# Optimization experiments

Measured on AMD Instinct MI355X. Metric: run time of the kernel, lower is better.

## Reference

```python
import jax, jax.numpy as jnp
import numpy as np

NUM_FEATURES = 256
NUM_PIDS = 5554          # must equal hardcoded FocalLoss ignore_index
NUM_CQ = 50000
N_ROIS = 2048
OIM_SCALAR = 30.0
IGNORE_INDEX = 5554
ALPHA = 1.0
GAMMA = 2.0


def _l2norm(x):
    return x / jnp.linalg.norm(x, axis=-1, keepdims=True)


def setup_inputs() -> dict:
    key = jax.random.key(0)
    k1, k2, k3, k4, k5 = jax.random.split(key, 5)
    inputs = _l2norm(jax.random.normal(k1, (N_ROIS, NUM_FEATURES), jnp.float32))
    # targets >= 1 so label = targets-1 >= 0 (the inds filter is all-True -> static shapes)
    # targets == NUM_PIDS+1 -> label == NUM_PIDS == ignore_index (unlabeled, ignored in loss)
    targets = jax.random.randint(k2, (N_ROIS,), 1, NUM_PIDS + 2, dtype=jnp.int64)
    ious = jax.random.uniform(k3, (N_ROIS,), jnp.float32)
    lut = _l2norm(jax.random.normal(k4, (NUM_PIDS, NUM_FEATURES), jnp.float32))
    cq = _l2norm(jax.random.normal(k5, (NUM_CQ, NUM_FEATURES), jnp.float32))
    return {"inputs": inputs, "lut": lut, "cq": cq, "targets": targets, "ious": ious}


def _focal_loss(logits, labels):
    # F.cross_entropy(reduction='none', ignore_index=IGNORE_INDEX) then
    # focal = alpha * (1-pt)^gamma * ce, mean over ALL samples (ignored -> 0).
    logp = jax.nn.log_softmax(logits, axis=-1)                       # [N, C]
    ce = -jnp.take_along_axis(logp, labels[:, None], axis=1)[:, 0]   # [N]
    ce = jnp.where(labels == IGNORE_INDEX, 0.0, ce)
    pt = jnp.exp(-ce)
    return jnp.mean(ALPHA * (1.0 - pt) ** GAMMA * ce)


def reference(inputs, lut, cq, targets, ious):
    # targets = cat(roi_label); label = targets - 1; inds all True by construction.
    label = targets - 1
    # LOIM forward: logits against labeled LUT and unlabeled circular queue.
    table = jnp.concatenate([lut, cq], axis=0)          # [P+Q, D]
    projected = OIM_SCALAR * (inputs @ table.T)         # [N, P+Q]
    loss_oim = _focal_loss(projected, label)
    return loss_oim, inputs, label
```

## Files before the change

### kernel.cpp

```cpp
#include <hip/hip_runtime.h>
#include <hip/hip_bf16.h>


#define NFEAT 256
#define NROIS 2048
#define NPIDS 5554
#define NCLS 55554
#define NCHUNKS 3473
#define NCH32 1737
#define NCLSP (NCH32 * 32)
#define S2F 43.280851226668906f
#define LN2F 0.6931471805599453f
#define LOFF 524289

typedef float f32x4 __attribute__((ext_vector_type(4)));
typedef short bf16x8 __attribute__((ext_vector_type(8)));
typedef unsigned short u16x8 __attribute__((ext_vector_type(8)));

#if __has_builtin(__builtin_amdgcn_exp2f)
#define EXP2(x) __builtin_amdgcn_exp2f(x)
#else
#define EXP2(x) exp2f(x)
#endif

__device__ __forceinline__ short bfb(float x) {
    return __builtin_bit_cast(short, __float2bfloat16(x));
}

__device__ __forceinline__ void gll16(const void* g, void* l) {
    __builtin_amdgcn_global_load_lds(
        (const __attribute__((address_space(1))) void*)g,
        (__attribute__((address_space(3))) void*)l, 16, 0, 0);
}

__global__ __launch_bounds__(256) void preprocess(
        const float* __restrict__ inputs, const float* __restrict__ lut,
        const float* __restrict__ cq, const int* __restrict__ cand0,
        const int* __restrict__ cand1, unsigned short* __restrict__ tb,
        unsigned short* __restrict__ ab, int* __restrict__ lab,
        float* __restrict__ S, float* __restrict__ f, const int useTB) {
    const int tid = threadIdx.x;
    const int bx = blockIdx.x;

    if (bx == 0) {
        __shared__ int smode;
        __shared__ const int* sT;
        if (tid == 0) {
            const int* T = cand0;
            const unsigned u0 = (unsigned)cand0[0];
            const float f0 = __builtin_bit_cast(float, cand0[0]);
            const bool oki = (u0 >= 1u && u0 <= 6000u);
            const bool okf = (f0 >= 1.0f && f0 <= 6000.0f);
            if (!oki && !okf) T = cand1;
            int mode = 0;
            const unsigned tu0 = (unsigned)T[0];
            const float tf0 = __builtin_bit_cast(float, T[0]);
            if (tu0 >= 1u && tu0 <= 6000u) mode = ((T[1] | T[3] | T[5] | T[7]) == 0) ? 1 : 0;
            else if (tf0 >= 1.0f && tf0 <= 6000.0f) mode = 2;
            smode = mode; sT = T;
        }
        __syncthreads();
        const int mode = smode;
        const int* T = sT;
        for (int j = tid; j < NROIS; j += 256) {
            int tv;
            if (mode == 1)      tv = T[2 * j];
            else if (mode == 2) tv = (int)__builtin_bit_cast(float, T[j]);
            else                tv = T[j];
            const int lv = tv - 1;
            lab[j] = lv;
            f[LOFF + j] = __bfloat162float(__float2bfloat16((float)lv));
        }
        for (int j = tid; j < NROIS + 8; j += 256) S[j] = 0.0f;
    }

    if (bx < 512) {
        const int i = bx * 256 + tid;
        const float4 v = *reinterpret_cast<const float4*>(inputs + (size_t)i * 4);
        float* o = f + 1 + (size_t)i * 4;
        o[0] = v.x; o[1] = v.y; o[2] = v.z; o[3] = v.w;
        if (useTB) {
            ushort4 u;
            u.x = (unsigned short)bfb(v.x); u.y = (unsigned short)bfb(v.y);
            u.z = (unsigned short)bfb(v.z); u.w = (unsigned short)bfb(v.w);
            *reinterpret_cast<ushort4*>(ab + (size_t)i * 4) = u;
        }
    }

    if (useTB) {
        const size_t LUTN = (size_t)NPIDS * NFEAT;
        const size_t TOT  = (size_t)NCLS * NFEAT;
        const size_t TOTP = (size_t)NCLSP * NFEAT;
        const size_t stride = (size_t)gridDim.x * 256 * 8;
        for (size_t e = ((size_t)bx * 256 + tid) * 8; e < TOTP; e += stride) {
            u16x8 o = {0, 0, 0, 0, 0, 0, 0, 0};
            if (e < TOT) {
                const float* sp = (e < LUTN) ? (lut + e) : (cq + (e - LUTN));
                const float4 a = *reinterpret_cast<const float4*>(sp);
                const float4 b = *reinterpret_cast<const float4*>(sp + 4);
                o[0] = (unsigned short)bfb(a.x); o[1] = (unsigned short)bfb(a.y);
                o[2] = (unsigned short)bfb(a.z); o[3] = (unsigned short)bfb(a.w);
                o[4] = (unsigned short)bfb(b.x); o[5] = (unsigned short)bfb(b.y);
                o[6] = (unsigned short)bfb(b.z); o[7] = (unsigned short)bfb(b.w);
            }
            *reinterpret_cast<u16x8*>(tb + e) = o;
        }
    }
}

template <bool TB>
__global__ __launch_bounds__(256, 2) void main_gemm4(const float* __restrict__ inputs,
                                                     const unsigned short* __restrict__ tb,
                                                     const unsigned short* __restrict__ ab,
                                                     const float* __restrict__ lut,
                                                     const float* __restrict__ cq,
                                                     float* __restrict__ S) {
    __shared__ short ldsb[3][8192];
    const int tid = threadIdx.x;
    const int lane = tid & 63;
    const int wave = tid >> 6;
    const int cs = blockIdx.x & 63;
    const int rg = blockIdx.x >> 6;
    const int rowbase = rg * 256 + wave * 64;
    const int li = lane & 15;
    const int q = lane >> 4;
    const int xorli = 4 * (li & 7);

    bf16x8 afrag[4][8];
    if constexpr (TB) {
        #pragma unroll
        for (int s = 0; s < 4; s++) {
            const unsigned short* rp = ab + (size_t)(rowbase + s * 16 + li) * NFEAT + q * 8;
            #pragma unroll
            for (int kc = 0; kc < 8; kc++)
                afrag[s][kc] = *reinterpret_cast<const bf16x8*>(rp + kc * 32);
        }
    } else {
        #pragma unroll
        for (int s = 0; s < 4; s++) {
            const float* rp = inputs + (size_t)(rowbase + s * 16 + li) * NFEAT + q * 8;
            #pragma unroll
            for (int kc = 0; kc < 8; kc++) {
                const float4 x0 = *reinterpret_cast<const float4*>(rp + kc * 32);
                const float4 x1 = *reinterpret_cast<const float4*>(rp + kc * 32 + 4);
                bf16x8 a;
                a[0] = bfb(x0.x); a[1] = bfb(x0.y); a[2] = bfb(x0.z); a[3] = bfb(x0.w);
                a[4] = bfb(x1.x); a[5] = bfb(x1.y); a[6] = bfb(x1.z); a[7] = bfb(x1.w);
                afrag[s][kc] = a;
            }
        }
    }

    float sums[4][4] = {{0.f,0.f,0.f,0.f},{0.f,0.f,0.f,0.f},
                        {0.f,0.f,0.f,0.f},{0.f,0.f,0.f,0.f}};
    char* const lbase = (char*)&ldsb[0][0];

    if constexpr (TB) {
        const int cc0 = tid >> 5;
        const int uo = ((tid & 31) ^ (4 * (cc0 & 7))) * 8;
        const int ldd = wave * 1024;
        const int cA = (cs * NCH32) >> 6;
        const int cB = ((cs + 1) * NCH32) >> 6;
        const int NB = cB - cA;
        const unsigned short* psrc = tb + (size_t)(cA * 32 + cc0) * NFEAT + uo;
        int ob0 = 0, ob1 = 16384, ob2 = 32768;

        #pragma unroll
        for (int k = 0; k < 4; k++)
            gll16(psrc + (size_t)(8 * k) * NFEAT, lbase + ob0 + ldd + k * 4096);
        psrc += (size_t)32 * NFEAT;
        if (NB > 1) {
            #pragma unroll
            for (int k = 0; k < 4; k++)
                gll16(psrc + (size_t)(8 * k) * NFEAT, lbase + ob1 + ldd + k * 4096);
            psrc += (size_t)32 * NFEAT;
        }

        for (int i = 0; i < NB; ++i) {
            if (i + 1 < NB) asm volatile("s_waitcnt vmcnt(4)\n\ts_barrier" ::: "memory");
            else            asm volatile("s_waitcnt vmcnt(0)\n\ts_barrier" ::: "memory");
            if (i + 2 < NB) {
                #pragma unroll
                for (int k = 0; k < 4; k++)
                    gll16(psrc + (size_t)(8 * k) * NFEAT, lbase + ob2 + ldd + k * 4096);
                psrc += (size_t)32 * NFEAT;
            }
            #pragma unroll
            for (int h = 0; h < 2; h++) {
                const int cc = h * 16 + li;
                bf16x8 bfr[8];
                #pragma unroll
                for (int kc = 0; kc < 8; kc++) {
                    const int slot = cc * 32 + ((q + 4 * kc) ^ xorli);
                    bfr[kc] = *reinterpret_cast<const bf16x8*>(lbase + ob0 + slot * 16);
                }
                f32x4 acc[4] = {{0.f,0.f,0.f,0.f},{0.f,0.f,0.f,0.f},
                                {0.f,0.f,0.f,0.f},{0.f,0.f,0.f,0.f}};
                __builtin_amdgcn_s_setprio(1);
                #pragma unroll
                for (int kc = 0; kc < 8; kc++) {
                    acc[0] = __builtin_amdgcn_mfma_f32_16x16x32_bf16(afrag[0][kc], bfr[kc], acc[0], 0, 0, 0);
                    acc[1] = __builtin_amdgcn_mfma_f32_16x16x32_bf16(afrag[1][kc], bfr[kc], acc[1], 0, 0, 0);
                    acc[2] = __builtin_amdgcn_mfma_f32_16x16x32_bf16(afrag[2][kc], bfr[kc], acc[2], 0, 0, 0);
                    acc[3] = __builtin_amdgcn_mfma_f32_16x16x32_bf16(afrag[3][kc], bfr[kc], acc[3], 0, 0, 0);
                }
                __builtin_amdgcn_s_setprio(0);
                #pragma unroll
                for (int s = 0; s < 4; s++)
                    #pragma unroll
                    for (int r = 0; r < 4; r++)
                        sums[s][r] += EXP2(S2F * acc[s][r] - S2F);
            }
            const int t = ob0; ob0 = ob1; ob1 = ob2; ob2 = t;
        }
    } else {
        short* fb = (short*)lbase;
        const int s0 = tid, s1 = tid + 256;
        const int cc0 = s0 >> 5, cc1 = s1 >> 5;
        const int uo0 = ((s0 & 31) ^ (4 * (cc0 & 7))) * 8;
        const int uo1 = ((s1 & 31) ^ (4 * (cc1 & 7))) * 8;
        const int cA = (cs * NCHUNKS) >> 6;
        const int cB = ((cs + 1) * NCHUNKS) >> 6;
        {
            int n0 = cA * 16 + cc0; n0 = n0 < (NCLS - 1) ? n0 : (NCLS - 1);
            int n1 = cA * 16 + cc1; n1 = n1 < (NCLS - 1) ? n1 : (NCLS - 1);
            const float* r0 = ((n0 < NPIDS) ? lut + (size_t)n0 * NFEAT
                                            : cq + (size_t)(n0 - NPIDS) * NFEAT) + uo0;
            const float* r1 = ((n1 < NPIDS) ? lut + (size_t)n1 * NFEAT
                                            : cq + (size_t)(n1 - NPIDS) * NFEAT) + uo1;
            const float4 a0 = *reinterpret_cast<const float4*>(r0);
            const float4 a1 = *reinterpret_cast<const float4*>(r0 + 4);
            const float4 b0 = *reinterpret_cast<const float4*>(r1);
            const float4 b1 = *reinterpret_cast<const float4*>(r1 + 4);
            bf16x8 v0, v1;
            v0[0]=bfb(a0.x); v0[1]=bfb(a0.y); v0[2]=bfb(a0.z); v0[3]=bfb(a0.w);
            v0[4]=bfb(a1.x); v0[5]=bfb(a1.y); v0[6]=bfb(a1.z); v0[7]=bfb(a1.w);
            v1[0]=bfb(b0.x); v1[1]=bfb(b0.y); v1[2]=bfb(b0.z); v1[3]=bfb(b0.w);
            v1[4]=bfb(b1.x); v1[5]=bfb(b1.y); v1[6]=bfb(b1.z); v1[7]=bfb(b1.w);
            *reinterpret_cast<bf16x8*>(&fb[s0 * 8]) = v0;
            *reinterpret_cast<bf16x8*>(&fb[s1 * 8]) = v1;
        }
        __syncthreads();
        int cur = 0;
        for (int ci = cA; ci < cB; ++ci) {
            const bool pf = (ci + 1 < cB);
            float4 f0a, f0b, f1a, f1b;
            if (pf) {
                int n0 = (ci + 1) * 16 + cc0; n0 = n0 < (NCLS - 1) ? n0 : (NCLS - 1);
                int n1 = (ci + 1) * 16 + cc1; n1 = n1 < (NCLS - 1) ? n1 : (NCLS - 1);
                const float* r0 = ((n0 < NPIDS) ? lut + (size_t)n0 * NFEAT
                                                : cq + (size_t)(n0 - NPIDS) * NFEAT) + uo0;
                const float* r1 = ((n1 < NPIDS) ? lut + (size_t)n1 * NFEAT
                                                : cq + (size_t)(n1 - NPIDS) * NFEAT) + uo1;
                f0a = *reinterpret_cast<const float4*>(r0);
                f0b = *reinterpret_cast<const float4*>(r0 + 4);
                f1a = *reinterpret_cast<const float4*>(r1);
                f1b = *reinterpret_cast<const float4*>(r1 + 4);
            }
            f32x4 acc[4] = {{0.f,0.f,0.f,0.f},{0.f,0.f,0.f,0.f},
                            {0.f,0.f,0.f,0.f},{0.f,0.f,0.f,0.f}};
            #pragma unroll
            for (int kc = 0; kc < 8; kc++) {
                const int slot = li * 32 + ((q + 4 * kc) ^ xorli);
                const bf16x8 b = *reinterpret_cast<const bf16x8*>(&fb[cur * 4096 + slot * 8]);
                acc[0] = __builtin_amdgcn_mfma_f32_16x16x32_bf16(afrag[0][kc], b, acc[0], 0, 0, 0);
                acc[1] = __builtin_amdgcn_mfma_f32_16x16x32_bf16(afrag[1][kc], b, acc[1], 0, 0, 0);
                acc[2] = __builtin_amdgcn_mfma_f32_16x16x32_bf16(afrag[2][kc], b, acc[2], 0, 0, 0);
                acc[3] = __builtin_amdgcn_mfma_f32_16x16x32_bf16(afrag[3][kc], b, acc[3], 0, 0, 0);
            }
            const float valid = ((ci * 16 + li) < NCLS) ? 1.0f : 0.0f;
            #pragma unroll
            for (int s = 0; s < 4; s++)
                #pragma unroll
                for (int r = 0; r < 4; r++)
                    sums[s][r] += valid * EXP2(S2F * (acc[s][r] - 1.0f));
            if (pf) {
                bf16x8 p0, p1;
                p0[0]=bfb(f0a.x); p0[1]=bfb(f0a.y); p0[2]=bfb(f0a.z); p0[3]=bfb(f0a.w);
                p0[4]=bfb(f0b.x); p0[5]=bfb(f0b.y); p0[6]=bfb(f0b.z); p0[7]=bfb(f0b.w);
                p1[0]=bfb(f1a.x); p1[1]=bfb(f1a.y); p1[2]=bfb(f1a.z); p1[3]=bfb(f1a.w);
                p1[4]=bfb(f1b.x); p1[5]=bfb(f1b.y); p1[6]=bfb(f1b.z); p1[7]=bfb(f1b.w);
                *reinterpret_cast<bf16x8*>(&fb[(cur ^ 1) * 4096 + s0 * 8]) = p0;
                *reinterpret_cast<bf16x8*>(&fb[(cur ^ 1) * 4096 + s1 * 8]) = p1;
            }
            __syncthreads();
            cur ^= 1;
        }
    }

    #pragma unroll
    for (int s = 0; s < 4; s++)
        #pragma unroll
        for (int r = 0; r < 4; r++) {
            float v = sums[s][r];
            v += __shfl_xor(v, 1); v += __shfl_xor(v, 2);
            v += __shfl_xor(v, 4); v += __shfl_xor(v, 8);
            sums[s][r] = v;
        }
    if (li == 0) {
        #pragma unroll
        for (int s = 0; s < 4; s++)
            #pragma unroll
            for (int r = 0; r < 4; r++)
                atomicAdd(&S[rowbase + s * 16 + q * 4 + r], sums[s][r]);
    }
}

__global__ __launch_bounds__(256) void focal_final(const float* __restrict__ inputs,
                                                   const float* __restrict__ lut,
                                                   const int* __restrict__ lab,
                                                   const float* __restrict__ S,
                                                   float* __restrict__ loss_acc,
                                                   unsigned int* __restrict__ cnt,
                                                   float* __restrict__ f) {
    const int wave = threadIdx.x >> 6;
    const int lane = threadIdx.x & 63;
    const int row = blockIdx.x * 4 + wave;
    const int label = lab[row];
    const bool valid = (label >= 0 && label < NPIDS);
    const int lr = valid ? label : 0;
    const float4 a = *reinterpret_cast<const float4*>(inputs + (size_t)row * NFEAT + lane * 4);
    const float4 b = *reinterpret_cast<const float4*>(lut + (size_t)lr * NFEAT + lane * 4);
    float v = a.x * b.x + a.y * b.y + a.z * b.z + a.w * b.w;
    #pragma unroll
    for (int m = 1; m < 64; m <<= 1) v += __shfl_xor(v, m);

    __shared__ float red[4];
    if (lane == 0) {
        float fo = 0.0f;
        if (valid) {
            const float l2 = v * S2F;
            const float lse2 = S2F + log2f(S[row]);
            float ce = fmaxf((lse2 - l2) * LN2F, 0.0f);
            const float pt = EXP2(l2 - lse2);
            const float om = 1.0f - pt;
            fo = om * om * ce;
        }
        red[wave] = fo;
    }
    __syncthreads();
    if (threadIdx.x == 0) {
        atomicAdd(loss_acc, red[0] + red[1] + red[2] + red[3]);
        __threadfence();
        const unsigned done = atomicAdd(cnt, 1u) + 1u;
        if (done == gridDim.x) {
            const float tot = atomicAdd(loss_acc, 0.0f);
            f[0] = tot * (1.0f / NROIS);
        }
    }
}

extern "C" void kernel_launch(void* const* d_in, const int* in_sizes, int n_in,
                              void* d_out, int out_size, void* d_ws, size_t ws_size,
                              hipStream_t stream) {
    const float* inputs = (const float*)d_in[0];
    const float* lut    = (const float*)d_in[1];
    const float* cq     = (const float*)d_in[2];
    const int*   cand0  = (const int*)d_in[3];
    const int*   cand1  = (const int*)((n_in > 4) ? d_in[4] : d_in[3]);
    float* f = (float*)d_out;

    const size_t TBB = (size_t)NCLSP * NFEAT * 2;
    const size_t ABB = (size_t)NROIS * NFEAT * 2;
    char* ws = (char*)d_ws;
    const bool useTB = ws_size >= TBB + ABB + 32768;

    unsigned short* tb = useTB ? (unsigned short*)ws : nullptr;
    unsigned short* ab = useTB ? (unsigned short*)(ws + TBB) : nullptr;
    float* S = useTB ? (float*)(ws + TBB + ABB) : (float*)ws;
    float* loss_acc    = S + NROIS;
    unsigned int* cnt  = (unsigned int*)(S + NROIS + 1);
    int* lab           = (int*)(S + NROIS + 8);

    preprocess<<<useTB ? 4096 : 512, 256, 0, stream>>>(inputs, lut, cq, cand0, cand1,
                                                       tb, ab, lab, S, f, useTB ? 1 : 0);
    if (useTB) main_gemm4<true><<<512, 256, 0, stream>>>(inputs, tb, ab, lut, cq, S);
    else       main_gemm4<false><<<512, 256, 0, stream>>>(inputs, tb, ab, lut, cq, S);
    focal_final<<<512, 256, 0, stream>>>(inputs, lut, lab, S, loss_acc, cnt, f);
}
```

Measured before the change: 171.5 us.

## Switch bf16 GEMM tile to 32x32x16 MFMA with new LDS swizzle

The workspace-backed path now uses 32x32x16 bf16 MFMA instructions instead of 16x16x32. Each wave holds two 32-row A fragments over 16 K-chunks, and the LDS XOR swizzle and B-fragment indexing are changed to match the new lane layout. The row-sum reduction is updated for 32-lane groups. This is meant to cut instruction count and LDS reads per FLOP, at the cost of more accumulator registers and different bank-conflict behaviour.

```diff
diff --git a/kernel.cpp b/kernel.cpp
--- a/kernel.cpp
+++ b/kernel.cpp
@@ -14,6 +14,7 @@
 #define LOFF 524289
 
 typedef float f32x4 __attribute__((ext_vector_type(4)));
+typedef float f32x16 __attribute__((ext_vector_type(16)));
 typedef short bf16x8 __attribute__((ext_vector_type(8)));
 typedef unsigned short u16x8 __attribute__((ext_vector_type(8)));
 
@@ -109,7 +110,7 @@
 }
 
 template <bool TB>
-__global__ __launch_bounds__(256, 2) void main_gemm4(const float* __restrict__ inputs,
+__global__ __launch_bounds__(256, 2) void main_gemm5(const float* __restrict__ inputs,
                                                      const unsigned short* __restrict__ tb,
                                                      const unsigned short* __restrict__ ab,
                                                      const float* __restrict__ lut,
@@ -122,20 +123,110 @@
     const int cs = blockIdx.x & 63;
     const int rg = blockIdx.x >> 6;
     const int rowbase = rg * 256 + wave * 64;
-    const int li = lane & 15;
-    const int q = lane >> 4;
-    const int xorli = 4 * (li & 7);
-
-    bf16x8 afrag[4][8];
+    char* const lbase = (char*)&ldsb[0][0];
+
     if constexpr (TB) {
-        #pragma unroll
-        for (int s = 0; s < 4; s++) {
-            const unsigned short* rp = ab + (size_t)(rowbase + s * 16 + li) * NFEAT + q * 8;
-            #pragma unroll
-            for (int kc = 0; kc < 8; kc++)
-                afrag[s][kc] = *reinterpret_cast<const bf16x8*>(rp + kc * 32);
+        const int cc = lane & 31;
+        const int p  = lane >> 5;
+        const int xc = 2 * (cc & 3);
+
+        bf16x8 afrag[2][16];
+        #pragma unroll
+        for (int s = 0; s < 2; s++) {
+            const unsigned short* rp = ab + (size_t)(rowbase + s * 32 + cc) * NFEAT + p * 8;
+            #pragma unroll
+            for (int kc = 0; kc < 16; kc++)
+                afrag[s][kc] = *reinterpret_cast<const bf16x8*>(rp + kc * 16);
+        }
+
+        float sums[2][16];
+        #pragma unroll
+        for (int s = 0; s < 2; s++)
+            #pragma unroll
+            for (int r = 0; r < 16; r++) sums[s][r] = 0.0f;
+
+        const int cc0 = tid >> 5;
+        const int uo = ((tid & 31) ^ (2 * (cc0 & 3))) * 8;
+        const int ldd = wave * 1024;
+        const int cA = (cs * NCH32) >> 6;
+        const int cB = ((cs + 1) * NCH32) >> 6;
+        const int NB = cB - cA;
+        const unsigned short* psrc = tb + (size_t)(cA * 32 + cc0) * NFEAT + uo;
+        int ob0 = 0, ob1 = 16384, ob2 = 32768;
+
+        #pragma unroll
+        for (int k = 0; k < 4; k++)
+            gll16(psrc + (size_t)(8 * k) * NFEAT, lbase + ob0 + ldd + k * 4096);
+        psrc += (size_t)32 * NFEAT;
+        if (NB > 1) {
+            #pragma unroll
+            for (int k = 0; k < 4; k++)
+                gll16(psrc + (size_t)(8 * k) * NFEAT, lbase + ob1 + ldd + k * 4096);
+            psrc += (size_t)32 * NFEAT;
+        }
+
+        for (int i = 0; i < NB; ++i) {
+            if (i + 1 < NB) asm volatile("s_waitcnt vmcnt(4)\n\ts_barrier" ::: "memory");
+            else            asm volatile("s_waitcnt vmcnt(0)\n\ts_barrier" ::: "memory");
+            if (i + 2 < NB) {
+                #pragma unroll
+                for (int k = 0; k < 4; k++)
+                    gll16(psrc + (size_t)(8 * k) * NFEAT, lbase + ob2 + ldd + k * 4096);
+                psrc += (size_t)32 * NFEAT;
+            }
+            f32x16 acc0 = {0.f,0.f,0.f,0.f,0.f,0.f,0.f,0.f,
+                           0.f,0.f,0.f,0.f,0.f,0.f,0.f,0.f};
+            f32x16 acc1 = {0.f,0.f,0.f,0.f,0.f,0.f,0.f,0.f,
+                           0.f,0.f,0.f,0.f,0.f,0.f,0.f,0.f};
+            #pragma unroll
+            for (int h = 0; h < 2; h++) {
+                bf16x8 bfr[8];
+                #pragma unroll
+                for (int j = 0; j < 8; j++) {
+                    const int kc = h * 8 + j;
+                    const int slot = cc * 32 + ((2 * kc + p) ^ xc);
+                    bfr[j] = *reinterpret_cast<const bf16x8*>(lbase + ob0 + slot * 16);
+                }
+                __builtin_amdgcn_s_setprio(1);
+                #pragma unroll
+                for (int j = 0; j < 8; j++) {
+                    acc0 = __builtin_amdgcn_mfma_f32_32x32x16_bf16(afrag[0][h * 8 + j], bfr[j], acc0, 0, 0, 0);
+                    acc1 = __builtin_amdgcn_mfma_f32_32x32x16_bf16(afrag[1][h * 8 + j], bfr[j], acc1, 0, 0, 0);
+                }
+                __builtin_amdgcn_s_setprio(0);
+            }
+            #pragma unroll
+            for (int r = 0; r < 16; r++) {
+                sums[0][r] += EXP2(S2F * acc0[r] - S2F);
+                sums[1][r] += EXP2(S2F * acc1[r] - S2F);
+            }
+            const int t = ob0; ob0 = ob1; ob1 = ob2; ob2 = t;
+        }
+
+        #pragma unroll
+        for (int s = 0; s < 2; s++)
+            #pragma unroll
+            for (int r = 0; r < 16; r++) {
+                float v = sums[s][r];
+                v += __shfl_xor(v, 1); v += __shfl_xor(v, 2);
+                v += __shfl_xor(v, 4); v += __shfl_xor(v, 8);
+                v += __shfl_xor(v, 16);
+                sums[s][r] = v;
+            }
+        if (cc == 0) {
+            #pragma unroll
+            for (int s = 0; s < 2; s++)
+                #pragma unroll
+                for (int r = 0; r < 16; r++) {
+                    const int row = rowbase + s * 32 + (r & 3) + 8 * (r >> 2) + 4 * p;
+                    atomicAdd(&S[row], sums[s][r]);
+                }
         }
     } else {
+        const int li = lane & 15;
+        const int q = lane >> 4;
+        const int xorli = 4 * (li & 7);
+        bf16x8 afrag[4][8];
         #pragma unroll
         for (int s = 0; s < 4; s++) {
             const float* rp = inputs + (size_t)(rowbase + s * 16 + li) * NFEAT + q * 8;
@@ -149,71 +240,8 @@
                 afrag[s][kc] = a;
             }
         }
-    }
-
-    float sums[4][4] = {{0.f,0.f,0.f,0.f},{0.f,0.f,0.f,0.f},
-                        {0.f,0.f,0.f,0.f},{0.f,0.f,0.f,0.f}};
-    char* const lbase = (char*)&ldsb[0][0];
-
-    if constexpr (TB) {
-        const int cc0 = tid >> 5;
-        const int uo = ((tid & 31) ^ (4 * (cc0 & 7))) * 8;
-        const int ldd = wave * 1024;
-        const int cA = (cs * NCH32) >> 6;
-        const int cB = ((cs + 1) * NCH32) >> 6;
-        const int NB = cB - cA;
-        const unsigned short* psrc = tb + (size_t)(cA * 32 + cc0) * NFEAT + uo;
-        int ob0 = 0, ob1 = 16384, ob2 = 32768;
-
-        #pragma unroll
-        for (int k = 0; k < 4; k++)
-            gll16(psrc + (size_t)(8 * k) * NFEAT, lbase + ob0 + ldd + k * 4096);
-        psrc += (size_t)32 * NFEAT;
-        if (NB > 1) {
-            #pragma unroll
-            for (int k = 0; k < 4; k++)
-                gll16(psrc + (size_t)(8 * k) * NFEAT, lbase + ob1 + ldd + k * 4096);
-            psrc += (size_t)32 * NFEAT;
-        }
-
-        for (int i = 0; i < NB; ++i) {
-            if (i + 1 < NB) asm volatile("s_waitcnt vmcnt(4)\n\ts_barrier" ::: "memory");
-            else            asm volatile("s_waitcnt vmcnt(0)\n\ts_barrier" ::: "memory");
-            if (i + 2 < NB) {
-                #pragma unroll
-                for (int k = 0; k < 4; k++)
-                    gll16(psrc + (size_t)(8 * k) * NFEAT, lbase + ob2 + ldd + k * 4096);
-                psrc += (size_t)32 * NFEAT;
-            }
-            #pragma unroll
-            for (int h = 0; h < 2; h++) {
-                const int cc = h * 16 + li;
-                bf16x8 bfr[8];
-                #pragma unroll
-                for (int kc = 0; kc < 8; kc++) {
-                    const int slot = cc * 32 + ((q + 4 * kc) ^ xorli);
-                    bfr[kc] = *reinterpret_cast<const bf16x8*>(lbase + ob0 + slot * 16);
-                }
-                f32x4 acc[4] = {{0.f,0.f,0.f,0.f},{0.f,0.f,0.f,0.f},
-                                {0.f,0.f,0.f,0.f},{0.f,0.f,0.f,0.f}};
-                __builtin_amdgcn_s_setprio(1);
-                #pragma unroll
-                for (int kc = 0; kc < 8; kc++) {
-                    acc[0] = __builtin_amdgcn_mfma_f32_16x16x32_bf16(afrag[0][kc], bfr[kc], acc[0], 0, 0, 0);
-                    acc[1] = __builtin_amdgcn_mfma_f32_16x16x32_bf16(afrag[1][kc], bfr[kc], acc[1], 0, 0, 0);
-                    acc[2] = __builtin_amdgcn_mfma_f32_16x16x32_bf16(afrag[2][kc], bfr[kc], acc[2], 0, 0, 0);
-                    acc[3] = __builtin_amdgcn_mfma_f32_16x16x32_bf16(afrag[3][kc], bfr[kc], acc[3], 0, 0, 0);
-                }
-                __builtin_amdgcn_s_setprio(0);
-                #pragma unroll
-                for (int s = 0; s < 4; s++)
-                    #pragma unroll
-                    for (int r = 0; r < 4; r++)
-                        sums[s][r] += EXP2(S2F * acc[s][r] - S2F);
-            }
-            const int t = ob0; ob0 = ob1; ob1 = ob2; ob2 = t;
-        }
-    } else {
+        float sums[4][4] = {{0.f,0.f,0.f,0.f},{0.f,0.f,0.f,0.f},
+                            {0.f,0.f,0.f,0.f},{0.f,0.f,0.f,0.f}};
         short* fb = (short*)lbase;
         const int s0 = tid, s1 = tid + 256;
         const int cc0 = s0 >> 5, cc1 = s1 >> 5;
@@ -286,23 +314,22 @@
             __syncthreads();
             cur ^= 1;
         }
-    }
-
-    #pragma unroll
-    for (int s = 0; s < 4; s++)
-        #pragma unroll
-        for (int r = 0; r < 4; r++) {
-            float v = sums[s][r];
-            v += __shfl_xor(v, 1); v += __shfl_xor(v, 2);
-            v += __shfl_xor(v, 4); v += __shfl_xor(v, 8);
-            sums[s][r] = v;
-        }
-    if (li == 0) {
         #pragma unroll
         for (int s = 0; s < 4; s++)
             #pragma unroll
-            for (int r = 0; r < 4; r++)
-                atomicAdd(&S[rowbase + s * 16 + q * 4 + r], sums[s][r]);
+            for (int r = 0; r < 4; r++) {
+                float v = sums[s][r];
+                v += __shfl_xor(v, 1); v += __shfl_xor(v, 2);
+                v += __shfl_xor(v, 4); v += __shfl_xor(v, 8);
+                sums[s][r] = v;
+            }
+        if (li == 0) {
+            #pragma unroll
+            for (int s = 0; s < 4; s++)
+                #pragma unroll
+                for (int r = 0; r < 4; r++)
+                    atomicAdd(&S[rowbase + s * 16 + q * 4 + r], sums[s][r]);
+        }
     }
 }
 
@@ -374,7 +401,7 @@
 
     preprocess<<<useTB ? 4096 : 512, 256, 0, stream>>>(inputs, lut, cq, cand0, cand1,
                                                        tb, ab, lab, S, f, useTB ? 1 : 0);
-    if (useTB) main_gemm4<true><<<512, 256, 0, stream>>>(inputs, tb, ab, lut, cq, S);
-    else       main_gemm4<false><<<512, 256, 0, stream>>>(inputs, tb, ab, lut, cq, S);
+    if (useTB) main_gemm5<true><<<512, 256, 0, stream>>>(inputs, tb, ab, lut, cq, S);
+    else       main_gemm5<false><<<512, 256, 0, stream>>>(inputs, tb, ab, lut, cq, S);
     focal_final<<<512, 256, 0, stream>>>(inputs, lut, lab, S, loss_acc, cnt, f);
 }
```

After: 190.8 us. 11.2% more time.

## Use 512-thread blocks with 32 rows per wave in fused GEMM

Applied to the files above, without the earlier changes.

The main GEMM+exp kernel now runs 8 waves per block, each owning 32 rows instead of 64. Each wave keeps half as many A fragments and accumulators, and the cooperative LDS loads are split across twice as many threads. The goal is to cut register pressure and raise occupancy (launch bounds 512,4) so latency is hidden better. The cost is that each LDS B-fragment read now feeds only 2 MFMAs instead of 4, which doubles LDS read traffic per FLOP and halves per-wave reuse.

```diff
diff --git a/kernel.cpp b/kernel.cpp
--- a/kernel.cpp
+++ b/kernel.cpp
@@ -109,7 +109,7 @@
 }
 
 template <bool TB>
-__global__ __launch_bounds__(256, 2) void main_gemm4(const float* __restrict__ inputs,
+__global__ __launch_bounds__(512, 4) void main_gemm6(const float* __restrict__ inputs,
                                                      const unsigned short* __restrict__ tb,
                                                      const unsigned short* __restrict__ ab,
                                                      const float* __restrict__ lut,
@@ -121,15 +121,16 @@
     const int wave = tid >> 6;
     const int cs = blockIdx.x & 63;
     const int rg = blockIdx.x >> 6;
-    const int rowbase = rg * 256 + wave * 64;
+    const int rowbase = rg * 256 + wave * 32;
     const int li = lane & 15;
     const int q = lane >> 4;
     const int xorli = 4 * (li & 7);
-
-    bf16x8 afrag[4][8];
+    char* const lbase = (char*)&ldsb[0][0];
+
+    bf16x8 afrag[2][8];
     if constexpr (TB) {
         #pragma unroll
-        for (int s = 0; s < 4; s++) {
+        for (int s = 0; s < 2; s++) {
             const unsigned short* rp = ab + (size_t)(rowbase + s * 16 + li) * NFEAT + q * 8;
             #pragma unroll
             for (int kc = 0; kc < 8; kc++)
@@ -137,7 +138,7 @@
         }
     } else {
         #pragma unroll
-        for (int s = 0; s < 4; s++) {
+        for (int s = 0; s < 2; s++) {
             const float* rp = inputs + (size_t)(rowbase + s * 16 + li) * NFEAT + q * 8;
             #pragma unroll
             for (int kc = 0; kc < 8; kc++) {
@@ -151,9 +152,7 @@
         }
     }
 
-    float sums[4][4] = {{0.f,0.f,0.f,0.f},{0.f,0.f,0.f,0.f},
-                        {0.f,0.f,0.f,0.f},{0.f,0.f,0.f,0.f}};
-    char* const lbase = (char*)&ldsb[0][0];
+    float sums[2][4] = {{0.f,0.f,0.f,0.f},{0.f,0.f,0.f,0.f}};
 
     if constexpr (TB) {
         const int cc0 = tid >> 5;
@@ -165,24 +164,21 @@
         const unsigned short* psrc = tb + (size_t)(cA * 32 + cc0) * NFEAT + uo;
         int ob0 = 0, ob1 = 16384, ob2 = 32768;
 
-        #pragma unroll
-        for (int k = 0; k < 4; k++)
-            gll16(psrc + (size_t)(8 * k) * NFEAT, lbase + ob0 + ldd + k * 4096);
+        gll16(psrc, lbase + ob0 + ldd);
+        gll16(psrc + (size_t)16 * NFEAT, lbase + ob0 + 8192 + ldd);
         psrc += (size_t)32 * NFEAT;
         if (NB > 1) {
-            #pragma unroll
-            for (int k = 0; k < 4; k++)
-                gll16(psrc + (size_t)(8 * k) * NFEAT, lbase + ob1 + ldd + k * 4096);
+            gll16(psrc, lbase + ob1 + ldd);
+            gll16(psrc + (size_t)16 * NFEAT, lbase + ob1 + 8192 + ldd);
             psrc += (size_t)32 * NFEAT;
         }
 
         for (int i = 0; i < NB; ++i) {
-            if (i + 1 < NB) asm volatile("s_waitcnt vmcnt(4)\n\ts_barrier" ::: "memory");
+            if (i + 1 < NB) asm volatile("s_waitcnt vmcnt(2)\n\ts_barrier" ::: "memory");
             else            asm volatile("s_waitcnt vmcnt(0)\n\ts_barrier" ::: "memory");
             if (i + 2 < NB) {
-                #pragma unroll
-                for (int k = 0; k < 4; k++)
-                    gll16(psrc + (size_t)(8 * k) * NFEAT, lbase + ob2 + ldd + k * 4096);
+                gll16(psrc, lbase + ob2 + ldd);
+                gll16(psrc + (size_t)16 * NFEAT, lbase + ob2 + 8192 + ldd);
                 psrc += (size_t)32 * NFEAT;
             }
             #pragma unroll
@@ -194,19 +190,16 @@
                     const int slot = cc * 32 + ((q + 4 * kc) ^ xorli);
                     bfr[kc] = *reinterpret_cast<const bf16x8*>(lbase + ob0 + slot * 16);
                 }
-                f32x4 acc[4] = {{0.f,0.f,0.f,0.f},{0.f,0.f,0.f,0.f},
-                                {0.f,0.f,0.f,0.f},{0.f,0.f,0.f,0.f}};
+                f32x4 acc[2] = {{0.f,0.f,0.f,0.f},{0.f,0.f,0.f,0.f}};
                 __builtin_amdgcn_s_setprio(1);
                 #pragma unroll
                 for (int kc = 0; kc < 8; kc++) {
                     acc[0] = __builtin_amdgcn_mfma_f32_16x16x32_bf16(afrag[0][kc], bfr[kc], acc[0], 0, 0, 0);
                     acc[1] = __builtin_amdgcn_mfma_f32_16x16x32_bf16(afrag[1][kc], bfr[kc], acc[1], 0, 0, 0);
-                    acc[2] = __builtin_amdgcn_mfma_f32_16x16x32_bf16(afrag[2][kc], bfr[kc], acc[2], 0, 0, 0);
-                    acc[3] = __builtin_amdgcn_mfma_f32_16x16x32_bf16(afrag[3][kc], bfr[kc], acc[3], 0, 0, 0);
                 }
                 __builtin_amdgcn_s_setprio(0);
                 #pragma unroll
-                for (int s = 0; s < 4; s++)
+                for (int s = 0; s < 2; s++)
                     #pragma unroll
                     for (int r = 0; r < 4; r++)
                         sums[s][r] += EXP2(S2F * acc[s][r] - S2F);
@@ -215,73 +208,52 @@
         }
     } else {
         short* fb = (short*)lbase;
-        const int s0 = tid, s1 = tid + 256;
-        const int cc0 = s0 >> 5, cc1 = s1 >> 5;
-        const int uo0 = ((s0 & 31) ^ (4 * (cc0 & 7))) * 8;
-        const int uo1 = ((s1 & 31) ^ (4 * (cc1 & 7))) * 8;
+        const int cc0 = tid >> 5;
+        const int uo0 = ((tid & 31) ^ (4 * (cc0 & 7))) * 8;
         const int cA = (cs * NCHUNKS) >> 6;
         const int cB = ((cs + 1) * NCHUNKS) >> 6;
         {
             int n0 = cA * 16 + cc0; n0 = n0 < (NCLS - 1) ? n0 : (NCLS - 1);
-            int n1 = cA * 16 + cc1; n1 = n1 < (NCLS - 1) ? n1 : (NCLS - 1);
             const float* r0 = ((n0 < NPIDS) ? lut + (size_t)n0 * NFEAT
                                             : cq + (size_t)(n0 - NPIDS) * NFEAT) + uo0;
-            const float* r1 = ((n1 < NPIDS) ? lut + (size_t)n1 * NFEAT
-                                            : cq + (size_t)(n1 - NPIDS) * NFEAT) + uo1;
             const float4 a0 = *reinterpret_cast<const float4*>(r0);
             const float4 a1 = *reinterpret_cast<const float4*>(r0 + 4);
-            const float4 b0 = *reinterpret_cast<const float4*>(r1);
-            const float4 b1 = *reinterpret_cast<const float4*>(r1 + 4);
-            bf16x8 v0, v1;
+            bf16x8 v0;
             v0[0]=bfb(a0.x); v0[1]=bfb(a0.y); v0[2]=bfb(a0.z); v0[3]=bfb(a0.w);
             v0[4]=bfb(a1.x); v0[5]=bfb(a1.y); v0[6]=bfb(a1.z); v0[7]=bfb(a1.w);
-            v1[0]=bfb(b0.x); v1[1]=bfb(b0.y); v1[2]=bfb(b0.z); v1[3]=bfb(b0.w);
-            v1[4]=bfb(b1.x); v1[5]=bfb(b1.y); v1[6]=bfb(b1.z); v1[7]=bfb(b1.w);
-            *reinterpret_cast<bf16x8*>(&fb[s0 * 8]) = v0;
-            *reinterpret_cast<bf16x8*>(&fb[s1 * 8]) = v1;
+            *reinterpret_cast<bf16x8*>(&fb[tid * 8]) = v0;
         }
         __syncthreads();
         int cur = 0;
         for (int ci = cA; ci < cB; ++ci) {
             const bool pf = (ci + 1 < cB);
-            float4 f0a, f0b, f1a, f1b;
+            float4 f0a, f0b;
             if (pf) {
                 int n0 = (ci + 1) * 16 + cc0; n0 = n0 < (NCLS - 1) ? n0 : (NCLS - 1);
-                int n1 = (ci + 1) * 16 + cc1; n1 = n1 < (NCLS - 1) ? n1 : (NCLS - 1);
                 const float* r0 = ((n0 < NPIDS) ? lut + (size_t)n0 * NFEAT
                                                 : cq + (size_t)(n0 - NPIDS) * NFEAT) + uo0;
-                const float* r1 = ((n1 < NPIDS) ? lut + (size_t)n1 * NFEAT
-                                                : cq + (size_t)(n1 - NPIDS) * NFEAT) + uo1;
                 f0a = *reinterpret_cast<const float4*>(r0);
                 f0b = *reinterpret_cast<const float4*>(r0 + 4);
-                f1a = *reinterpret_cast<const float4*>(r1);
-                f1b = *reinterpret_cast<const float4*>(r1 + 4);
-            }
-            f32x4 acc[4] = {{0.f,0.f,0.f,0.f},{0.f,0.f,0.f,0.f},
-                            {0.f,0.f,0.f,0.f},{0.f,0.f,0.f,0.f}};
+            }
+            f32x4 acc[2] = {{0.f,0.f,0.f,0.f},{0.f,0.f,0.f,0.f}};
             #pragma unroll
             for (int kc = 0; kc < 8; kc++) {
                 const int slot = li * 32 + ((q + 4 * kc) ^ xorli);
                 const bf16x8 b = *reinterpret_cast<const bf16x8*>(&fb[cur * 4096 + slot * 8]);
                 acc[0] = __builtin_amdgcn_mfma_f32_16x16x32_bf16(afrag[0][kc], b, acc[0], 0, 0, 0);
                 acc[1] = __builtin_amdgcn_mfma_f32_16x16x32_bf16(afrag[1][kc], b, acc[1], 0, 0, 0);
-                acc[2] = __builtin_amdgcn_mfma_f32_16x16x32_bf16(afrag[2][kc], b, acc[2], 0, 0, 0);
-                acc[3] = __builtin_amdgcn_mfma_f32_16x16x32_bf16(afrag[3][kc], b, acc[3], 0, 0, 0);
             }
             const float valid = ((ci * 16 + li) < NCLS) ? 1.0f : 0.0f;
             #pragma unroll
-            for (int s = 0; s < 4; s++)
+            for (int s = 0; s < 2; s++)
                 #pragma unroll
                 for (int r = 0; r < 4; r++)
                     sums[s][r] += valid * EXP2(S2F * (acc[s][r] - 1.0f));
             if (pf) {
-                bf16x8 p0, p1;
+                bf16x8 p0;
                 p0[0]=bfb(f0a.x); p0[1]=bfb(f0a.y); p0[2]=bfb(f0a.z); p0[3]=bfb(f0a.w);
                 p0[4]=bfb(f0b.x); p0[5]=bfb(f0b.y); p0[6]=bfb(f0b.z); p0[7]=bfb(f0b.w);
-                p1[0]=bfb(f1a.x); p1[1]=bfb(f1a.y); p1[2]=bfb(f1a.z); p1[3]=bfb(f1a.w);
-                p1[4]=bfb(f1b.x); p1[5]=bfb(f1b.y); p1[6]=bfb(f1b.z); p1[7]=bfb(f1b.w);
-                *reinterpret_cast<bf16x8*>(&fb[(cur ^ 1) * 4096 + s0 * 8]) = p0;
-                *reinterpret_cast<bf16x8*>(&fb[(cur ^ 1) * 4096 + s1 * 8]) = p1;
+                *reinterpret_cast<bf16x8*>(&fb[(cur ^ 1) * 4096 + tid * 8]) = p0;
             }
             __syncthreads();
             cur ^= 1;
@@ -289,7 +261,7 @@
     }
 
     #pragma unroll
-    for (int s = 0; s < 4; s++)
+    for (int s = 0; s < 2; s++)
         #pragma unroll
         for (int r = 0; r < 4; r++) {
             float v = sums[s][r];
@@ -299,7 +271,7 @@
         }
     if (li == 0) {
         #pragma unroll
-        for (int s = 0; s < 4; s++)
+        for (int s = 0; s < 2; s++)
             #pragma unroll
             for (int r = 0; r < 4; r++)
                 atomicAdd(&S[rowbase + s * 16 + q * 4 + r], sums[s][r]);
@@ -374,7 +346,7 @@
 
     preprocess<<<useTB ? 4096 : 512, 256, 0, stream>>>(inputs, lut, cq, cand0, cand1,
                                                        tb, ab, lab, S, f, useTB ? 1 : 0);
-    if (useTB) main_gemm4<true><<<512, 256, 0, stream>>>(inputs, tb, ab, lut, cq, S);
-    else       main_gemm4<false><<<512, 256, 0, stream>>>(inputs, tb, ab, lut, cq, S);
+    if (useTB) main_gemm6<true><<<512, 512, 0, stream>>>(inputs, tb, ab, lut, cq, S);
+    else       main_gemm6<false><<<512, 512, 0, stream>>>(inputs, tb, ab, lut, cq, S);
     focal_final<<<512, 256, 0, stream>>>(inputs, lut, lab, S, loss_acc, cnt, f);
 }
```

Result: slower. 185.9 us (+8.4%).

## Fuse preprocess, GEMM and focal reduction into one cooperative kernel

Applied to the files above, without the earlier changes.

Replaces the three separate launches (bf16 conversion, GEMM with exp-sum, focal finalize) with a single cooperative kernel that uses grid-wide syncs between phases. The aim is to remove kernel launch gaps and the tail idle time between dependent kernels. In exchange, the conversion phase now runs on only 512 blocks instead of 4096, and grid syncs carry their own cost. If the cooperative launch fails, the code falls back to the old three-kernel path.

```diff
diff --git a/kernel.cpp b/kernel.cpp
--- a/kernel.cpp
+++ b/kernel.cpp
@@ -1,5 +1,8 @@
 #include <hip/hip_runtime.h>
 #include <hip/hip_bf16.h>
+#include <hip/hip_cooperative_groups.h>
+
+namespace cg = cooperative_groups;
 
 
 #define NFEAT 256
@@ -33,14 +36,18 @@
         (__attribute__((address_space(3))) void*)l, 16, 0, 0);
 }
 
-__global__ __launch_bounds__(256) void preprocess(
+__global__ __launch_bounds__(256, 2) void mega(
         const float* __restrict__ inputs, const float* __restrict__ lut,
         const float* __restrict__ cq, const int* __restrict__ cand0,
         const int* __restrict__ cand1, unsigned short* __restrict__ tb,
         unsigned short* __restrict__ ab, int* __restrict__ lab,
-        float* __restrict__ S, float* __restrict__ f, const int useTB) {
+        float* __restrict__ S, float* __restrict__ loss_acc,
+        unsigned int* __restrict__ cnt, float* __restrict__ f) {
+    __shared__ short ldsb[3][8192];
     const int tid = threadIdx.x;
     const int bx = blockIdx.x;
+    const int lane = tid & 63;
+    const int wave = tid >> 6;
 
     if (bx == 0) {
         __shared__ int smode;
@@ -73,7 +80,212 @@
         }
         for (int j = tid; j < NROIS + 8; j += 256) S[j] = 0.0f;
     }
-
+    {
+        const int i = bx * 256 + tid;
+        const float4 v = *reinterpret_cast<const float4*>(inputs + (size_t)i * 4);
+        float* o = f + 1 + (size_t)i * 4;
+        o[0] = v.x; o[1] = v.y; o[2] = v.z; o[3] = v.w;
+        ushort4 u;
+        u.x = (unsigned short)bfb(v.x); u.y = (unsigned short)bfb(v.y);
+        u.z = (unsigned short)bfb(v.z); u.w = (unsigned short)bfb(v.w);
+        *reinterpret_cast<ushort4*>(ab + (size_t)i * 4) = u;
+    }
+    {
+        const size_t LUTN = (size_t)NPIDS * NFEAT;
+        const size_t TOT  = (size_t)NCLS * NFEAT;
+        const size_t TOTP = (size_t)NCLSP * NFEAT;
+        const size_t stride = (size_t)gridDim.x * 256 * 8;
+        for (size_t e = ((size_t)bx * 256 + tid) * 8; e < TOTP; e += stride) {
+            u16x8 o = {0, 0, 0, 0, 0, 0, 0, 0};
+            if (e < TOT) {
+                const float* sp = (e < LUTN) ? (lut + e) : (cq + (e - LUTN));
+                const float4 a = *reinterpret_cast<const float4*>(sp);
+                const float4 b = *reinterpret_cast<const float4*>(sp + 4);
+                o[0] = (unsigned short)bfb(a.x); o[1] = (unsigned short)bfb(a.y);
+                o[2] = (unsigned short)bfb(a.z); o[3] = (unsigned short)bfb(a.w);
+                o[4] = (unsigned short)bfb(b.x); o[5] = (unsigned short)bfb(b.y);
+                o[6] = (unsigned short)bfb(b.z); o[7] = (unsigned short)bfb(b.w);
+            }
+            *reinterpret_cast<u16x8*>(tb + e) = o;
+        }
+    }
+    cg::this_grid().sync();
+
+    {
+        const int cs = bx & 63;
+        const int rg = bx >> 6;
+        const int rowbase = rg * 256 + wave * 64;
+        const int li = lane & 15;
+        const int q = lane >> 4;
+        const int xorli = 4 * (li & 7);
+        char* const lbase = (char*)&ldsb[0][0];
+
+        bf16x8 afrag[4][8];
+        #pragma unroll
+        for (int s = 0; s < 4; s++) {
+            const unsigned short* rp = ab + (size_t)(rowbase + s * 16 + li) * NFEAT + q * 8;
+            #pragma unroll
+            for (int kc = 0; kc < 8; kc++)
+                afrag[s][kc] = *reinterpret_cast<const bf16x8*>(rp + kc * 32);
+        }
+
+        float sums[4][4] = {{0.f,0.f,0.f,0.f},{0.f,0.f,0.f,0.f},
+                            {0.f,0.f,0.f,0.f},{0.f,0.f,0.f,0.f}};
+
+        const int cc0 = tid >> 5;
+        const int uo = ((tid & 31) ^ (4 * (cc0 & 7))) * 8;
+        const int ldd = wave * 1024;
+        const int cA = (cs * NCH32) >> 6;
+        const int cB = ((cs + 1) * NCH32) >> 6;
+        const int NB = cB - cA;
+        const unsigned short* psrc = tb + (size_t)(cA * 32 + cc0) * NFEAT + uo;
+        int ob0 = 0, ob1 = 16384, ob2 = 32768;
+
+        #pragma unroll
+        for (int k = 0; k < 4; k++)
+            gll16(psrc + (size_t)(8 * k) * NFEAT, lbase + ob0 + ldd + k * 4096);
+        psrc += (size_t)32 * NFEAT;
+        if (NB > 1) {
+            #pragma unroll
+            for (int k = 0; k < 4; k++)
+                gll16(psrc + (size_t)(8 * k) * NFEAT, lbase + ob1 + ldd + k * 4096);
+            psrc += (size_t)32 * NFEAT;
+        }
+
+        for (int i = 0; i < NB; ++i) {
+            if (i + 1 < NB) asm volatile("s_waitcnt vmcnt(4)\n\ts_barrier" ::: "memory");
+            else            asm volatile("s_waitcnt vmcnt(0)\n\ts_barrier" ::: "memory");
+            if (i + 2 < NB) {
+                #pragma unroll
+                for (int k = 0; k < 4; k++)
+                    gll16(psrc + (size_t)(8 * k) * NFEAT, lbase + ob2 + ldd + k * 4096);
+                psrc += (size_t)32 * NFEAT;
+            }
+            #pragma unroll
+            for (int h = 0; h < 2; h++) {
+                const int cc = h * 16 + li;
+                bf16x8 bfr[8];
+                #pragma unroll
+                for (int kc = 0; kc < 8; kc++) {
+                    const int slot = cc * 32 + ((q + 4 * kc) ^ xorli);
+                    bfr[kc] = *reinterpret_cast<const bf16x8*>(lbase + ob0 + slot * 16);
+                }
+                f32x4 acc[4] = {{0.f,0.f,0.f,0.f},{0.f,0.f,0.f,0.f},
+                                {0.f,0.f,0.f,0.f},{0.f,0.f,0.f,0.f}};
+                __builtin_amdgcn_s_setprio(1);
+                #pragma unroll
+                for (int kc = 0; kc < 8; kc++) {
+                    acc[0] = __builtin_amdgcn_mfma_f32_16x16x32_bf16(afrag[0][kc], bfr[kc], acc[0], 0, 0, 0);
+                    acc[1] = __builtin_amdgcn_mfma_f32_16x16x32_bf16(afrag[1][kc], bfr[kc], acc[1], 0, 0, 0);
+                    acc[2] = __builtin_amdgcn_mfma_f32_16x16x32_bf16(afrag[2][kc], bfr[kc], acc[2], 0, 0, 0);
+                    acc[3] = __builtin_amdgcn_mfma_f32_16x16x32_bf16(afrag[3][kc], bfr[kc], acc[3], 0, 0, 0);
+                }
+                __builtin_amdgcn_s_setprio(0);
+                #pragma unroll
+                for (int s = 0; s < 4; s++)
+                    #pragma unroll
+                    for (int r = 0; r < 4; r++)
+                        sums[s][r] += EXP2(S2F * acc[s][r] - S2F);
+            }
+            const int t = ob0; ob0 = ob1; ob1 = ob2; ob2 = t;
+        }
+
+        #pragma unroll
+        for (int s = 0; s < 4; s++)
+            #pragma unroll
+            for (int r = 0; r < 4; r++) {
+                float v = sums[s][r];
+                v += __shfl_xor(v, 1); v += __shfl_xor(v, 2);
+                v += __shfl_xor(v, 4); v += __shfl_xor(v, 8);
+                sums[s][r] = v;
+            }
+        if (li == 0) {
+            #pragma unroll
+            for (int s = 0; s < 4; s++)
+                #pragma unroll
+                for (int r = 0; r < 4; r++)
+                    atomicAdd(&S[rowbase + s * 16 + q * 4 + r], sums[s][r]);
+        }
+    }
+    cg::this_grid().sync();
+
+    {
+        const int row = bx * 4 + wave;
+        const int label = lab[row];
+        const bool valid = (label >= 0 && label < NPIDS);
+        const int lr = valid ? label : 0;
+        const float4 a = *reinterpret_cast<const float4*>(inputs + (size_t)row * NFEAT + lane * 4);
+        const float4 b = *reinterpret_cast<const float4*>(lut + (size_t)lr * NFEAT + lane * 4);
+        float v = a.x * b.x + a.y * b.y + a.z * b.z + a.w * b.w;
+        #pragma unroll
+        for (int m = 1; m < 64; m <<= 1) v += __shfl_xor(v, m);
+
+        __shared__ float red[4];
+        if (lane == 0) {
+            float fo = 0.0f;
+            if (valid) {
+                const float l2 = v * S2F;
+                const float lse2 = S2F + log2f(S[row]);
+                float ce = fmaxf((lse2 - l2) * LN2F, 0.0f);
+                const float pt = EXP2(l2 - lse2);
+                const float om = 1.0f - pt;
+                fo = om * om * ce;
+            }
+            red[wave] = fo;
+        }
+        __syncthreads();
+        if (tid == 0) {
+            atomicAdd(loss_acc, red[0] + red[1] + red[2] + red[3]);
+            __threadfence();
+            const unsigned done = atomicAdd(cnt, 1u) + 1u;
+            if (done == gridDim.x) {
+                const float tot = atomicAdd(loss_acc, 0.0f);
+                f[0] = tot * (1.0f / NROIS);
+            }
+        }
+    }
+}
+
+
+__global__ __launch_bounds__(256) void preprocess(
+        const float* __restrict__ inputs, const float* __restrict__ lut,
+        const float* __restrict__ cq, const int* __restrict__ cand0,
+        const int* __restrict__ cand1, unsigned short* __restrict__ tb,
+        unsigned short* __restrict__ ab, int* __restrict__ lab,
+        float* __restrict__ S, float* __restrict__ f, const int useTB) {
+    const int tid = threadIdx.x;
+    const int bx = blockIdx.x;
+    if (bx == 0) {
+        __shared__ int smode;
+        __shared__ const int* sT;
+        if (tid == 0) {
+            const int* T = cand0;
+            const unsigned u0 = (unsigned)cand0[0];
+            const float f0 = __builtin_bit_cast(float, cand0[0]);
+            const bool oki = (u0 >= 1u && u0 <= 6000u);
+            const bool okf = (f0 >= 1.0f && f0 <= 6000.0f);
+            if (!oki && !okf) T = cand1;
+            int mode = 0;
+            const unsigned tu0 = (unsigned)T[0];
+            const float tf0 = __builtin_bit_cast(float, T[0]);
+            if (tu0 >= 1u && tu0 <= 6000u) mode = ((T[1] | T[3] | T[5] | T[7]) == 0) ? 1 : 0;
+            else if (tf0 >= 1.0f && tf0 <= 6000.0f) mode = 2;
+            smode = mode; sT = T;
+        }
+        __syncthreads();
+        const int mode = smode;
+        const int* T = sT;
+        for (int j = tid; j < NROIS; j += 256) {
+            int tv;
+            if (mode == 1)      tv = T[2 * j];
+            else if (mode == 2) tv = (int)__builtin_bit_cast(float, T[j]);
+            else                tv = T[j];
+            const int lv = tv - 1;
+            lab[j] = lv;
+            f[LOFF + j] = __bfloat162float(__float2bfloat16((float)lv));
+        }
+        for (int j = tid; j < NROIS + 8; j += 256) S[j] = 0.0f;
+    }
     if (bx < 512) {
         const int i = bx * 256 + tid;
         const float4 v = *reinterpret_cast<const float4*>(inputs + (size_t)i * 4);
@@ -86,7 +298,6 @@
             *reinterpret_cast<ushort4*>(ab + (size_t)i * 4) = u;
         }
     }
-
     if (useTB) {
         const size_t LUTN = (size_t)NPIDS * NFEAT;
         const size_t TOT  = (size_t)NCLS * NFEAT;
@@ -372,6 +583,15 @@
     unsigned int* cnt  = (unsigned int*)(S + NROIS + 1);
     int* lab           = (int*)(S + NROIS + 8);
 
+    if (useTB) {
+        void* kargs[] = {(void*)&inputs, (void*)&lut, (void*)&cq, (void*)&cand0,
+                         (void*)&cand1, (void*)&tb, (void*)&ab, (void*)&lab,
+                         (void*)&S, (void*)&loss_acc, (void*)&cnt, (void*)&f};
+        const hipError_t ce = hipLaunchCooperativeKernel(
+            (const void*)mega, dim3(512), dim3(256), kargs, 0, stream);
+        if (ce == hipSuccess) return;
+    }
+
     preprocess<<<useTB ? 4096 : 512, 256, 0, stream>>>(inputs, lut, cq, cand0, cand1,
                                                        tb, ab, lab, S, f, useTB ? 1 : 0);
     if (useTB) main_gemm4<true><<<512, 256, 0, stream>>>(inputs, tb, ab, lut, cq, S);
```

Measured after the change: 315.0 us. 1.84x slower.
